# Performance work log

Hardware: AMD Instinct MI355X
Metric: run time of the kernel (lower is better)

Reference implementation:

```python
import jax, jax.numpy as jnp
import numpy as np

N = 40000; E = 640000; F_IN = 128; HID = 32; HEADS = 4; G = 64
NEG_SLOPE = 0.2; LN_EPS = 1e-5


def setup_inputs() -> dict:
    key = jax.random.key(0)
    ks = jax.random.split(key, 24)
    rn = lambda k, shape, s=0.1: jax.random.normal(k, shape, jnp.float32) * s
    d = {}
    d["x"] = jax.random.normal(ks[0], (N, F_IN), jnp.float32)
    d["edge_index"] = jax.random.randint(ks[1], (2, E), 0, N)
    d["batch"] = jnp.sort(jax.random.randint(ks[2], (N,), 0, G))
    # GAT layer 0: in F_IN -> HID per head, HEADS heads, concat
    d["W0"] = rn(ks[3], (F_IN, HEADS * HID))
    d["as0"] = rn(ks[4], (HEADS, HID)); d["ad0"] = rn(ks[5], (HEADS, HID))
    d["b0"] = jnp.zeros((HEADS * HID,), jnp.float32)
    d["ln0_g"] = jnp.ones((HEADS * HID,), jnp.float32); d["ln0_b"] = jnp.zeros((HEADS * HID,), jnp.float32)
    # GAT layer 1: HEADS*HID -> HID per head, HEADS heads, concat
    d["W1"] = rn(ks[6], (HEADS * HID, HEADS * HID))
    d["as1"] = rn(ks[7], (HEADS, HID)); d["ad1"] = rn(ks[8], (HEADS, HID))
    d["b1"] = jnp.zeros((HEADS * HID,), jnp.float32)
    d["ln1_g"] = jnp.ones((HEADS * HID,), jnp.float32); d["ln1_b"] = jnp.zeros((HEADS * HID,), jnp.float32)
    # GAT layer 2: HEADS*HID -> HID, 1 head, no concat
    d["W2"] = rn(ks[9], (HEADS * HID, HID))
    d["as2"] = rn(ks[10], (1, HID)); d["ad2"] = rn(ks[11], (1, HID))
    d["b2"] = jnp.zeros((HID,), jnp.float32)
    d["ln2_g"] = jnp.ones((HID,), jnp.float32); d["ln2_b"] = jnp.zeros((HID,), jnp.float32)
    # classifier: HID -> HID//2 -> 2
    d["fc1_w"] = rn(ks[12], (HID, HID // 2)); d["fc1_b"] = jnp.zeros((HID // 2,), jnp.float32)
    d["fc2_w"] = rn(ks[13], (HID // 2, 2)); d["fc2_b"] = jnp.zeros((2,), jnp.float32)
    return d


def gat_layer(x, src, dst, W, a_s, a_d, b, heads, out_c, concat):
    n = x.shape[0]
    h = (x @ W).reshape(n, heads, out_c)            # [N,H,C]
    al_s = jnp.sum(h * a_s, axis=-1)                # [N,H]
    al_d = jnp.sum(h * a_d, axis=-1)                # [N,H]
    e = jax.nn.leaky_relu(al_s[src] + al_d[dst], NEG_SLOPE)  # [E,H]
    m = jax.ops.segment_max(e, dst, num_segments=n)          # segment softmax over dst
    ex = jnp.exp(e - m[dst])
    s = jax.ops.segment_sum(ex, dst, num_segments=n)
    alpha = ex / (s[dst] + 1e-16)                   # [E,H]
    out = jax.ops.segment_sum(h[src] * alpha[:, :, None], dst, num_segments=n)  # [N,H,C]
    out = out.reshape(n, heads * out_c) if concat else out.mean(axis=1)
    return out + b


def layer_norm(x, g, b):
    mu = x.mean(-1, keepdims=True)
    var = jnp.var(x, axis=-1, keepdims=True)
    return (x - mu) * jax.lax.rsqrt(var + LN_EPS) * g + b


def reference(x, edge_index, batch, W0, as0, ad0, b0, ln0_g, ln0_b, W1, as1, ad1, b1, ln1_g, ln1_b, W2, as2, ad2, b2, ln2_g, ln2_b, fc1_w, fc1_b, fc2_w, fc2_b):
    src, dst = edge_index[0], edge_index[1]
    h = gat_layer(x, src, dst, W0, as0, ad0, b0, HEADS, HID, True)
    h = jax.nn.elu(layer_norm(h, ln0_g, ln0_b))
    h = gat_layer(h, src, dst, W1, as1, ad1, b1, HEADS, HID, True)
    h = jax.nn.elu(layer_norm(h, ln1_g, ln1_b))
    h = gat_layer(h, src, dst, W2, as2, ad2, b2, 1, HID, False)
    h = jax.nn.elu(layer_norm(h, ln2_g, ln2_b))
    cnt = jax.ops.segment_sum(jnp.ones((h.shape[0],), h.dtype), batch, num_segments=G)
    hg = jax.ops.segment_sum(h, batch, num_segments=G) / jnp.maximum(cnt, 1.0)[:, None]  # global mean pool [G,HID]
    z = jax.nn.relu(hg @ fc1_w + fc1_b)
    return z @ fc2_w + fc2_b
```

## Files before the change

kernel.cpp:

```cpp
#include <hip/hip_runtime.h>
#include <hip/hip_fp16.h>
#include <math.h>

#define NN 40000
#define EE 640000
#define NG 64
#define SCAN_BLOCKS ((NN + 1023) / 1024)

__device__ __forceinline__ float eluf(float x) { return x > 0.f ? x : expm1f(x); }

typedef const __attribute__((address_space(1))) char gas_char;
typedef __attribute__((address_space(3))) char las_char;

__device__ __forceinline__ void async_copy16(void* l, const void* g) {
  __builtin_amdgcn_global_load_lds((gas_char*)g, (las_char*)l, 16, 0, 0);
}

typedef __fp16 f16x2 __attribute__((ext_vector_type(2)));
__device__ __forceinline__ unsigned packh(float lo, float hi) {
  f16x2 p = __builtin_amdgcn_cvt_pkrtz(lo, hi);
  union { f16x2 h; unsigned u; } c; c.h = p; return c.u;
}
__device__ __forceinline__ float hlo(unsigned p) {
  union { unsigned u; f16x2 h; } c; c.u = p; return (float)c.h.x;
}
__device__ __forceinline__ float hhi(unsigned p) {
  union { unsigned u; f16x2 h; } c; c.u = p; return (float)c.h.y;
}

__global__ void zero_int_kernel(int* __restrict__ p, int n) {
  int i = blockIdx.x * 256 + threadIdx.x;
  if (i < n) p[i] = 0;
}

__global__ void count_deg_kernel(const int* __restrict__ dst, int* __restrict__ deg, int e) {
  int i = blockIdx.x * 256 + threadIdx.x;
  if (i < e) atomicAdd(&deg[dst[i]], 1);
}

__global__ __launch_bounds__(1024) void scanA_kernel(const int* __restrict__ deg,
                                                     int* __restrict__ row_ptr,
                                                     int* __restrict__ bsum, int n) {
  __shared__ int wsum[16];
  int t = threadIdx.x, lane = t & 63, wid = t >> 6;
  int i = blockIdx.x * 1024 + t;
  int v = (i < n) ? deg[i] : 0;
#pragma unroll
  for (int off = 1; off < 64; off <<= 1) {
    int u = __shfl_up(v, off);
    if (lane >= off) v += u;
  }
  if (lane == 63) wsum[wid] = v;
  __syncthreads();
  if (t < 16) {
    int w = wsum[t];
#pragma unroll
    for (int off = 1; off < 16; off <<= 1) {
      int u = __shfl_up(w, off);
      if (t >= off) w += u;
    }
    wsum[t] = w;
  }
  __syncthreads();
  if (wid > 0) v += wsum[wid - 1];
  if (i < n) row_ptr[i + 1] = v;
  if (t == 1023) bsum[blockIdx.x] = v;
}

__global__ void scanB_kernel(const int* __restrict__ bsum, int* __restrict__ boff, int nb) {
  int lane = threadIdx.x;
  int v = (lane < nb) ? bsum[lane] : 0;
  int orig = v;
#pragma unroll
  for (int off = 1; off < 64; off <<= 1) {
    int u = __shfl_up(v, off);
    if (lane >= off) v += u;
  }
  if (lane < nb) boff[lane] = v - orig;
}

__global__ __launch_bounds__(1024) void scanC_kernel(int* __restrict__ row_ptr,
                                                     const int* __restrict__ boff,
                                                     int* __restrict__ cursor, int n) {
  int i = blockIdx.x * 1024 + threadIdx.x;
  if (i < n) {
    int v = row_ptr[i + 1] + boff[i >> 10];
    row_ptr[i + 1] = v;
    if (i + 1 < n) cursor[i + 1] = v;
    if (i == 0) { cursor[0] = 0; row_ptr[0] = 0; }
  }
}

__global__ void scatter_kernel(const int* __restrict__ src, const int* __restrict__ dst,
                               int* __restrict__ cursor, int* __restrict__ csr_src, int e) {
  int i = blockIdx.x * 256 + threadIdx.x;
  if (i < e) {
    int d = dst[i];
    int pos = atomicAdd(&cursor[d], 1);
    csr_src[pos] = src[i];
  }
}

__global__ __launch_bounds__(256, 2) void gemm128_kernel(
    const float* __restrict__ x, const float* __restrict__ W,
    const float* __restrict__ a_s, const float* __restrict__ a_d,
    unsigned* __restrict__ hb, float* __restrict__ als, float* __restrict__ ald)
{
  __shared__ float xs[64 * 128];
  __shared__ float ws[2][32 * 128];

  int t = threadIdx.x;
  int row0 = blockIdx.x * 64;

  {
    const char* xg = (const char*)(x + (size_t)row0 * 128);
    char* xl = (char*)xs;
#pragma unroll
    for (int it = 0; it < 8; ++it)
      async_copy16(xl + it * 4096 + t * 16, xg + it * 4096 + t * 16);
  }
  {
    const char* wg = (const char*)W;
    char* wl = (char*)ws[0];
#pragma unroll
    for (int p = 0; p < 4; ++p)
      async_copy16(wl + p * 4096 + t * 16, wg + p * 4096 + t * 16);
  }
  __syncthreads();

  int cg = t & 31, rg = t >> 5;
  int r0 = rg * 8;
  int jlo = 2 * cg;

  float acc[8][4];
#pragma unroll
  for (int r = 0; r < 8; ++r)
#pragma unroll
    for (int c = 0; c < 4; ++c) acc[r][c] = 0.f;

  for (int ch = 0; ch < 4; ++ch) {
    if (ch < 3) {
      const char* wg = (const char*)W + (size_t)(ch + 1) * 32 * 128 * 4;
      char* wl = (char*)ws[(ch + 1) & 1];
#pragma unroll
      for (int p = 0; p < 4; ++p)
        async_copy16(wl + p * 4096 + t * 16, wg + p * 4096 + t * 16);
    }
    const float* wc = ws[ch & 1];
    const float* xc = xs + ch * 32;
#pragma unroll
    for (int kk = 0; kk < 32; kk += 4) {
      float2 wlo[4], whi[4];
#pragma unroll
      for (int q = 0; q < 4; ++q) {
        wlo[q] = *reinterpret_cast<const float2*>(&wc[(kk + q) * 128 + jlo]);
        whi[q] = *reinterpret_cast<const float2*>(&wc[(kk + q) * 128 + 64 + jlo]);
      }
#pragma unroll
      for (int r = 0; r < 8; ++r) {
        float4 xv = *reinterpret_cast<const float4*>(&xc[(r0 + r) * 128 + kk]);
        float a0 = acc[r][0], a1 = acc[r][1], a2 = acc[r][2], a3 = acc[r][3];
        a0 = fmaf(xv.x, wlo[0].x, a0); a1 = fmaf(xv.x, wlo[0].y, a1);
        a2 = fmaf(xv.x, whi[0].x, a2); a3 = fmaf(xv.x, whi[0].y, a3);
        a0 = fmaf(xv.y, wlo[1].x, a0); a1 = fmaf(xv.y, wlo[1].y, a1);
        a2 = fmaf(xv.y, whi[1].x, a2); a3 = fmaf(xv.y, whi[1].y, a3);
        a0 = fmaf(xv.z, wlo[2].x, a0); a1 = fmaf(xv.z, wlo[2].y, a1);
        a2 = fmaf(xv.z, whi[2].x, a2); a3 = fmaf(xv.z, whi[2].y, a3);
        a0 = fmaf(xv.w, wlo[3].x, a0); a1 = fmaf(xv.w, wlo[3].y, a1);
        a2 = fmaf(xv.w, whi[3].x, a2); a3 = fmaf(xv.w, whi[3].y, a3);
        acc[r][0] = a0; acc[r][1] = a1; acc[r][2] = a2; acc[r][3] = a3;
      }
    }
    __syncthreads();
  }

#pragma unroll
  for (int r = 0; r < 8; ++r) {
    uint2 pv;
    pv.x = packh(acc[r][0], acc[r][2]);
    pv.y = packh(acc[r][1], acc[r][3]);
    *reinterpret_cast<uint2*>(&hb[(size_t)(row0 + r0 + r) * 64 + jlo]) = pv;
  }

  float as0 = a_s[jlo], as1 = a_s[jlo + 1], as2 = a_s[jlo + 64], as3 = a_s[jlo + 65];
  float ad0 = a_d[jlo], ad1 = a_d[jlo + 1], ad2 = a_d[jlo + 64], ad3 = a_d[jlo + 65];
  int lane = t & 63;
#pragma unroll
  for (int r = 0; r < 8; ++r) {
    float psa = fmaf(acc[r][0], as0, acc[r][1] * as1);
    float psb = fmaf(acc[r][2], as2, acc[r][3] * as3);
    float pda = fmaf(acc[r][0], ad0, acc[r][1] * ad1);
    float pdb = fmaf(acc[r][2], ad2, acc[r][3] * ad3);
#pragma unroll
    for (int m = 1; m < 16; m <<= 1) {
      psa += __shfl_xor(psa, m); psb += __shfl_xor(psb, m);
      pda += __shfl_xor(pda, m); pdb += __shfl_xor(pdb, m);
    }
    if ((lane & 15) == 0) {
      int hA = (lane >> 4) & 1;
      size_t row = (size_t)(row0 + r0 + r);
      als[row * 4 + hA] = psa; als[row * 4 + hA + 2] = psb;
      ald[row * 4 + hA] = pda; ald[row * 4 + hA + 2] = pdb;
    }
  }
}

__global__ __launch_bounds__(256, 2) void gemm32_kernel(
    const float* __restrict__ x, const float* __restrict__ W,
    const float* __restrict__ a_s, const float* __restrict__ a_d,
    float* __restrict__ h, float* __restrict__ als, float* __restrict__ ald)
{
  __shared__ float xs[64 * 128];
  __shared__ float ws[2][32 * 32];
  int t = threadIdx.x;
  int row0 = blockIdx.x * 64;
  {
    const char* xg = (const char*)(x + (size_t)row0 * 128);
    char* xl = (char*)xs;
#pragma unroll
    for (int it = 0; it < 8; ++it)
      async_copy16(xl + it * 4096 + t * 16, xg + it * 4096 + t * 16);
  }
  async_copy16((char*)ws[0] + t * 16, (const char*)W + t * 16);
  __syncthreads();

  int cg = t & 7, rg = t >> 3;
  int r0 = rg * 2, c0 = cg * 4;
  float acc[2][4];
#pragma unroll
  for (int r = 0; r < 2; ++r)
#pragma unroll
    for (int c = 0; c < 4; ++c) acc[r][c] = 0.f;

  for (int ch = 0; ch < 4; ++ch) {
    if (ch < 3) {
      const char* wg = (const char*)W + (size_t)(ch + 1) * 32 * 32 * 4;
      async_copy16((char*)ws[(ch + 1) & 1] + t * 16, wg + t * 16);
    }
    const float* wc = ws[ch & 1];
    const float* xc = xs + ch * 32;
#pragma unroll
    for (int kk = 0; kk < 32; kk += 4) {
      float4 wv[4];
#pragma unroll
      for (int q = 0; q < 4; ++q)
        wv[q] = *reinterpret_cast<const float4*>(&wc[(kk + q) * 32 + c0]);
#pragma unroll
      for (int r = 0; r < 2; ++r) {
        float4 xv = *reinterpret_cast<const float4*>(&xc[(r0 + r) * 128 + kk]);
#pragma unroll
        for (int c = 0; c < 4; ++c) {
          float a = acc[r][c];
          a = fmaf(xv.x, (&wv[0].x)[c], a);
          a = fmaf(xv.y, (&wv[1].x)[c], a);
          a = fmaf(xv.z, (&wv[2].x)[c], a);
          a = fmaf(xv.w, (&wv[3].x)[c], a);
          acc[r][c] = a;
        }
      }
    }
    __syncthreads();
  }

#pragma unroll
  for (int r = 0; r < 2; ++r) {
    float4 hv = make_float4(acc[r][0], acc[r][1], acc[r][2], acc[r][3]);
    *reinterpret_cast<float4*>(&h[(size_t)(row0 + r0 + r) * 32 + c0]) = hv;
  }
  float asv[4], adv[4];
#pragma unroll
  for (int c = 0; c < 4; ++c) { asv[c] = a_s[c0 + c]; adv[c] = a_d[c0 + c]; }
#pragma unroll
  for (int r = 0; r < 2; ++r) {
    float ps = acc[r][0] * asv[0] + acc[r][1] * asv[1] + acc[r][2] * asv[2] + acc[r][3] * asv[3];
    float pd = acc[r][0] * adv[0] + acc[r][1] * adv[1] + acc[r][2] * adv[2] + acc[r][3] * adv[3];
#pragma unroll
    for (int m = 1; m < 8; m <<= 1) { ps += __shfl_xor(ps, m); pd += __shfl_xor(pd, m); }
    if ((t & 7) == 0) {
      als[row0 + r0 + r] = ps;
      ald[row0 + r0 + r] = pd;
    }
  }
}

__global__ __launch_bounds__(256) void aggregate128_kernel(
    const unsigned* __restrict__ hb, const float* __restrict__ als, const float* __restrict__ ald,
    const int* __restrict__ row_ptr, const int* __restrict__ csr_src,
    const float* __restrict__ bias, const float* __restrict__ ln_g, const float* __restrict__ ln_b,
    float* __restrict__ out, int n)
{
  __shared__ int s_src[4][64];
  __shared__ float s_ex[4][64][4];
  int t = threadIdx.x, lane = t & 63, wid = t >> 6;
  int node = blockIdx.x * 4 + wid;
  if (node >= n) return;
  int start = row_ptr[node], end = row_ptr[node + 1];
  int deg = end - start;

  float4 adq = reinterpret_cast<const float4*>(ald)[node];
  float adl[4] = {adq.x, adq.y, adq.z, adq.w};
  int hi = lane >> 5, c = lane & 31;
  int h0 = c >> 4, h1 = h0 + 2;
  float a0 = 0.f, a1 = 0.f, a2 = 0.f, a3 = 0.f;
  float ssum[4];

  if (deg <= 64) {
    bool valid = lane < deg;
    int s = 0;
    if (valid) s = csr_src[start + lane];
    float4 q = reinterpret_cast<const float4*>(als)[s];
    float v[4] = {q.x, q.y, q.z, q.w};
    float ex[4];
#pragma unroll
    for (int hh = 0; hh < 4; ++hh) {
      float w = v[hh] + adl[hh];
      w = w > 0.f ? w : 0.2f * w;
      ex[hh] = valid ? __expf(w) : 0.f;
      ssum[hh] = ex[hh];
    }
#pragma unroll
    for (int hh = 0; hh < 4; ++hh)
#pragma unroll
      for (int m = 1; m < 64; m <<= 1) ssum[hh] += __shfl_xor(ssum[hh], m);

    s_src[wid][lane] = s;
#pragma unroll
    for (int hh = 0; hh < 4; ++hh) s_ex[wid][lane][hh] = ex[hh];

    int d1 = deg >> 1, d0c = deg - d1;
    int base = hi ? d0c : 0;
    int cnt = hi ? d1 : d0c;
    float b0a = 0.f, b1a = 0.f, b2a = 0.f, b3a = 0.f;
    int j = 0;
    for (; j + 2 <= cnt; j += 2) {
      int sa = s_src[wid][base + j];
      int sb = s_src[wid][base + j + 1];
      uint2 ua = *reinterpret_cast<const uint2*>(&hb[(size_t)sa * 64 + 2 * c]);
      uint2 ub = *reinterpret_cast<const uint2*>(&hb[(size_t)sb * 64 + 2 * c]);
      float wa0 = s_ex[wid][base + j][h0], wa1 = s_ex[wid][base + j][h1];
      float wb0 = s_ex[wid][base + j + 1][h0], wb1 = s_ex[wid][base + j + 1][h1];
      a0 = fmaf(wa0, hlo(ua.x), a0); a1 = fmaf(wa0, hlo(ua.y), a1);
      a2 = fmaf(wa1, hhi(ua.x), a2); a3 = fmaf(wa1, hhi(ua.y), a3);
      b0a = fmaf(wb0, hlo(ub.x), b0a); b1a = fmaf(wb0, hlo(ub.y), b1a);
      b2a = fmaf(wb1, hhi(ub.x), b2a); b3a = fmaf(wb1, hhi(ub.y), b3a);
    }
    if (j < cnt) {
      int sa = s_src[wid][base + j];
      uint2 ua = *reinterpret_cast<const uint2*>(&hb[(size_t)sa * 64 + 2 * c]);
      float wa0 = s_ex[wid][base + j][h0], wa1 = s_ex[wid][base + j][h1];
      a0 = fmaf(wa0, hlo(ua.x), a0); a1 = fmaf(wa0, hlo(ua.y), a1);
      a2 = fmaf(wa1, hhi(ua.x), a2); a3 = fmaf(wa1, hhi(ua.y), a3);
    }
    a0 += b0a; a1 += b1a; a2 += b2a; a3 += b3a;
    a0 += __shfl_xor(a0, 32); a1 += __shfl_xor(a1, 32);
    a2 += __shfl_xor(a2, 32); a3 += __shfl_xor(a3, 32);
  } else {
#pragma unroll
    for (int hh = 0; hh < 4; ++hh) ssum[hh] = 0.f;
    for (int eb = start; eb < end; eb += 64) {
      int e = eb + lane;
      int s = 0;
      float exv[4] = {0.f, 0.f, 0.f, 0.f};
      if (e < end) {
        s = csr_src[e];
        float4 q = reinterpret_cast<const float4*>(als)[s];
        float av[4] = {q.x, q.y, q.z, q.w};
#pragma unroll
        for (int hh = 0; hh < 4; ++hh) {
          float v = av[hh] + adl[hh];
          v = v > 0.f ? v : 0.2f * v;
          exv[hh] = __expf(v);
          ssum[hh] += exv[hh];
        }
      }
      s_src[wid][lane] = s;
#pragma unroll
      for (int hh = 0; hh < 4; ++hh) s_ex[wid][lane][hh] = exv[hh];
      int cnt = end - eb; if (cnt > 64) cnt = 64;
      for (int j = 0; j < cnt; ++j) {
        int sj = s_src[wid][j];
        uint2 u = *reinterpret_cast<const uint2*>(&hb[(size_t)sj * 64 + 2 * c]);
        float w0 = s_ex[wid][j][h0], w1 = s_ex[wid][j][h1];
        a0 = fmaf(w0, hlo(u.x), a0); a1 = fmaf(w0, hlo(u.y), a1);
        a2 = fmaf(w1, hhi(u.x), a2); a3 = fmaf(w1, hhi(u.y), a3);
      }
    }
#pragma unroll
    for (int hh = 0; hh < 4; ++hh)
#pragma unroll
      for (int m = 1; m < 64; m <<= 1) ssum[hh] += __shfl_xor(ssum[hh], m);
    a0 *= 0.5f; a1 *= 0.5f; a2 *= 0.5f; a3 *= 0.5f;
    a0 += __shfl_xor(a0, 32); a1 += __shfl_xor(a1, 32);
    a2 += __shfl_xor(a2, 32); a3 += __shfl_xor(a3, 32);
  }

  float2 blo = *reinterpret_cast<const float2*>(&bias[2 * c]);
  float2 bhi = *reinterpret_cast<const float2*>(&bias[2 * c + 64]);
  float is0 = 1.f / (ssum[h0] + 1e-16f), is1 = 1.f / (ssum[h1] + 1e-16f);
  float o0 = a0 * is0 + blo.x;
  float o1 = a1 * is0 + blo.y;
  float o2 = a2 * is1 + bhi.x;
  float o3 = a3 * is1 + bhi.y;
  float red = o0 + o1 + o2 + o3;
  float sq2 = o0 * o0 + o1 * o1 + o2 * o2 + o3 * o3;
#pragma unroll
  for (int m = 1; m < 64; m <<= 1) {
    red += __shfl_xor(red, m);
    sq2 += __shfl_xor(sq2, m);
  }
  float mu = red * (1.f / 256.f);
  float var = sq2 * (1.f / 256.f) - mu * mu;
  float rstd = rsqrtf(var + 1e-5f);
  int f = 2 * c + 64 * hi;
  float2 gv = *reinterpret_cast<const float2*>(&ln_g[f]);
  float2 bv = *reinterpret_cast<const float2*>(&ln_b[f]);
  float dx = (hi ? o2 : o0) - mu, dy = (hi ? o3 : o1) - mu;
  float2 yv;
  yv.x = eluf(dx * rstd * gv.x + bv.x);
  yv.y = eluf(dy * rstd * gv.y + bv.y);
  *reinterpret_cast<float2*>(&out[(size_t)node * 128 + f]) = yv;
}

__global__ __launch_bounds__(256) void aggregate32_kernel(
    const float* __restrict__ h, const float* __restrict__ als, const float* __restrict__ ald,
    const int* __restrict__ row_ptr, const int* __restrict__ csr_src,
    const float* __restrict__ bias, const float* __restrict__ ln_g, const float* __restrict__ ln_b,
    float* __restrict__ out, int n)
{
  __shared__ int s_src[4][64];
  __shared__ float s_ex[4][64];
  int t = threadIdx.x, lane = t & 63, wid = t >> 6;
  int node = blockIdx.x * 4 + wid;
  if (node >= n) return;
  int start = row_ptr[node], end = row_ptr[node + 1];
  int deg = end - start;
  float adl = ald[node];
  int hi = lane >> 5, col = lane & 31;
  float acc0 = 0.f, ssum = 0.f;

  if (deg <= 64) {
    bool valid = lane < deg;
    int s = 0;
    if (valid) s = csr_src[start + lane];
    float v = als[s] + adl;
    v = v > 0.f ? v : 0.2f * v;
    float ex = valid ? __expf(v) : 0.f;
    ssum = ex;
#pragma unroll
    for (int m = 1; m < 64; m <<= 1) ssum += __shfl_xor(ssum, m);
    s_src[wid][lane] = s;
    s_ex[wid][lane] = ex;

    int d1 = deg >> 1, d0c = deg - d1;
    int base = hi ? d0c : 0;
    int cnt = hi ? d1 : d0c;
    float acc1 = 0.f;
    int j = 0;
    for (; j + 2 <= cnt; j += 2) {
      int sa = s_src[wid][base + j];
      int sb = s_src[wid][base + j + 1];
      float ha = h[(size_t)sa * 32 + col];
      float hbv = h[(size_t)sb * 32 + col];
      acc0 = fmaf(s_ex[wid][base + j], ha, acc0);
      acc1 = fmaf(s_ex[wid][base + j + 1], hbv, acc1);
    }
    if (j < cnt)
      acc0 = fmaf(s_ex[wid][base + j], h[(size_t)s_src[wid][base + j] * 32 + col], acc0);
    acc0 += acc1;
    acc0 += __shfl_xor(acc0, 32);
  } else {
    for (int eb = start; eb < end; eb += 64) {
      int e = eb + lane;
      int s = 0; float ex = 0.f;
      if (e < end) {
        s = csr_src[e];
        float v = als[s] + adl;
        v = v > 0.f ? v : 0.2f * v;
        ex = __expf(v);
        ssum += ex;
      }
      s_src[wid][lane] = s;
      s_ex[wid][lane] = ex;
      int cnt = end - eb; if (cnt > 64) cnt = 64;
      for (int j = 0; j < cnt; ++j)
        acc0 = fmaf(s_ex[wid][j], h[(size_t)s_src[wid][j] * 32 + col], acc0);
    }
#pragma unroll
    for (int m = 1; m < 64; m <<= 1) ssum += __shfl_xor(ssum, m);
    acc0 *= 0.5f;
    acc0 += __shfl_xor(acc0, 32);
  }

  float o0 = acc0 / (ssum + 1e-16f) + bias[col];
  float red = o0, sq2 = o0 * o0;
#pragma unroll
  for (int m = 1; m < 64; m <<= 1) {
    red += __shfl_xor(red, m);
    sq2 += __shfl_xor(sq2, m);
  }
  float mu = red * (1.f / 64.f);
  float var = sq2 * (1.f / 64.f) - mu * mu;
  float rstd = rsqrtf(var + 1e-5f);
  float y0 = (o0 - mu) * rstd * ln_g[col] + ln_b[col];
  if (lane < 32) out[(size_t)node * 32 + col] = eluf(y0);
}

__device__ __forceinline__ int lower_bound_dev(const int* a, int n, int key) {
  int lo = 0, hi = n;
  while (lo < hi) { int mid = (lo + hi) >> 1; if (a[mid] < key) lo = mid + 1; else hi = mid; }
  return lo;
}

__global__ __launch_bounds__(256) void poolfc_kernel(
    const float* __restrict__ x2, const int* __restrict__ batch,
    const float* __restrict__ fc1w, const float* __restrict__ fc1b,
    const float* __restrict__ fc2w, const float* __restrict__ fc2b,
    float* __restrict__ out, int n)
{
  int g = blockIdx.x;
  int lo = lower_bound_dev(batch, n, g);
  int hi = lower_bound_dev(batch, n, g + 1);
  int t = threadIdx.x;
  int c = t & 31, r = t >> 5;
  float acc = 0.f;
  for (int i = lo + r; i < hi; i += 8) acc += x2[(size_t)i * 32 + c];
  __shared__ float red[8][32];
  __shared__ float hgl[32];
  __shared__ float zl[16];
  red[r][c] = acc;
  __syncthreads();
  if (r == 0) {
    float s = 0.f;
#pragma unroll
    for (int k = 0; k < 8; ++k) s += red[k][c];
    float cnt = (float)(hi - lo);
    hgl[c] = s / fmaxf(cnt, 1.f);
  }
  __syncthreads();
  if (t < 16) {
    float a = fc1b[t];
#pragma unroll
    for (int k = 0; k < 32; ++k) a = fmaf(hgl[k], fc1w[k * 16 + t], a);
    zl[t] = fmaxf(a, 0.f);
  }
  __syncthreads();
  if (t < 2) {
    float a = fc2b[t];
#pragma unroll
    for (int j = 0; j < 16; ++j) a = fmaf(zl[j], fc2w[j * 2 + t], a);
    out[g * 2 + t] = a;
  }
}

extern "C" void kernel_launch(void* const* d_in, const int* in_sizes, int n_in,
                              void* d_out, int out_size, void* d_ws, size_t ws_size,
                              hipStream_t stream) {
  const float* x    = (const float*)d_in[0];
  const int*   ei   = (const int*)d_in[1];
  const int*   batch= (const int*)d_in[2];
  const float* W0   = (const float*)d_in[3];
  const float* as0  = (const float*)d_in[4];
  const float* ad0  = (const float*)d_in[5];
  const float* b0   = (const float*)d_in[6];
  const float* ln0g = (const float*)d_in[7];
  const float* ln0b = (const float*)d_in[8];
  const float* W1   = (const float*)d_in[9];
  const float* as1  = (const float*)d_in[10];
  const float* ad1  = (const float*)d_in[11];
  const float* b1   = (const float*)d_in[12];
  const float* ln1g = (const float*)d_in[13];
  const float* ln1b = (const float*)d_in[14];
  const float* W2   = (const float*)d_in[15];
  const float* as2  = (const float*)d_in[16];
  const float* ad2  = (const float*)d_in[17];
  const float* b2   = (const float*)d_in[18];
  const float* ln2g = (const float*)d_in[19];
  const float* ln2b = (const float*)d_in[20];
  const float* fc1w = (const float*)d_in[21];
  const float* fc1b = (const float*)d_in[22];
  const float* fc2w = (const float*)d_in[23];
  const float* fc2b = (const float*)d_in[24];
  float* out = (float*)d_out;

  const int* srce = ei;
  const int* dste = ei + EE;

  unsigned* hb = (unsigned*)d_ws;
  float* B2  = (float*)(hb + (size_t)NN * 64);
  float* als = B2 + (size_t)NN * 128;
  float* ald = als + (size_t)NN * 4;
  float* h2  = ald + (size_t)NN * 4;
  float* x2  = h2 + (size_t)NN * 32;
  int* deg      = (int*)(x2 + (size_t)NN * 32);
  int* row_ptr  = deg + NN;
  int* cursor   = row_ptr + NN + 1;
  int* csr_src  = cursor + NN;
  int* bsum     = csr_src + EE;
  int* boff     = bsum + SCAN_BLOCKS;

  zero_int_kernel<<<(NN + 255) / 256, 256, 0, stream>>>(deg, NN);
  count_deg_kernel<<<(EE + 255) / 256, 256, 0, stream>>>(dste, deg, EE);
  scanA_kernel<<<SCAN_BLOCKS, 1024, 0, stream>>>(deg, row_ptr, bsum, NN);
  scanB_kernel<<<1, 64, 0, stream>>>(bsum, boff, SCAN_BLOCKS);
  scanC_kernel<<<SCAN_BLOCKS, 1024, 0, stream>>>(row_ptr, boff, cursor, NN);
  scatter_kernel<<<(EE + 255) / 256, 256, 0, stream>>>(srce, dste, cursor, csr_src, EE);

  gemm128_kernel<<<625, 256, 0, stream>>>(x, W0, as0, ad0, hb, als, ald);
  aggregate128_kernel<<<(NN + 3) / 4, 256, 0, stream>>>(hb, als, ald, row_ptr, csr_src,
                                                        b0, ln0g, ln0b, B2, NN);
  gemm128_kernel<<<625, 256, 0, stream>>>(B2, W1, as1, ad1, hb, als, ald);
  aggregate128_kernel<<<(NN + 3) / 4, 256, 0, stream>>>(hb, als, ald, row_ptr, csr_src,
                                                        b1, ln1g, ln1b, B2, NN);
  gemm32_kernel<<<625, 256, 0, stream>>>(B2, W2, as2, ad2, h2, als, ald);
  aggregate32_kernel<<<(NN + 3) / 4, 256, 0, stream>>>(h2, als, ald, row_ptr, csr_src,
                                                       b2, ln2g, ln2b, x2, NN);
  poolfc_kernel<<<NG, 256, 0, stream>>>(x2, batch, fc1w, fc1b, fc2w, fc2b, out, NN);
}
```

Measured before the change: 278.0 us.

## Stream x tiles through double-buffered LDS and fold softmax sums into aggregation loops

```diff
diff --git a/kernel.cpp b/kernel.cpp
--- a/kernel.cpp
+++ b/kernel.cpp
@@ -101,30 +101,26 @@
   }
 }
 
-__global__ __launch_bounds__(256, 2) void gemm128_kernel(
+__global__ __launch_bounds__(256, 3) void gemm128_kernel(
     const float* __restrict__ x, const float* __restrict__ W,
     const float* __restrict__ a_s, const float* __restrict__ a_d,
     unsigned* __restrict__ hb, float* __restrict__ als, float* __restrict__ ald)
 {
-  __shared__ float xs[64 * 128];
+  __shared__ float xs[2][64 * 32];
   __shared__ float ws[2][32 * 128];
 
   int t = threadIdx.x;
   int row0 = blockIdx.x * 64;
+  const char* xgb = (const char*)x + (size_t)row0 * 512;
 
   {
-    const char* xg = (const char*)(x + (size_t)row0 * 128);
-    char* xl = (char*)xs;
-#pragma unroll
-    for (int it = 0; it < 8; ++it)
-      async_copy16(xl + it * 4096 + t * 16, xg + it * 4096 + t * 16);
-  }
-  {
+    int li0 = t, li1 = t + 256;
+    async_copy16((char*)xs[0] + li0 * 16, xgb + (li0 >> 3) * 512 + (li0 & 7) * 16);
+    async_copy16((char*)xs[0] + li1 * 16, xgb + (li1 >> 3) * 512 + (li1 & 7) * 16);
     const char* wg = (const char*)W;
-    char* wl = (char*)ws[0];
 #pragma unroll
     for (int p = 0; p < 4; ++p)
-      async_copy16(wl + p * 4096 + t * 16, wg + p * 4096 + t * 16);
+      async_copy16((char*)ws[0] + p * 4096 + t * 16, wg + p * 4096 + t * 16);
   }
   __syncthreads();
 
@@ -140,14 +136,18 @@
 
   for (int ch = 0; ch < 4; ++ch) {
     if (ch < 3) {
+      int b = (ch + 1) & 1;
+      int li0 = t, li1 = t + 256;
+      const char* xg = xgb + (ch + 1) * 128;
+      async_copy16((char*)xs[b] + li0 * 16, xg + (li0 >> 3) * 512 + (li0 & 7) * 16);
+      async_copy16((char*)xs[b] + li1 * 16, xg + (li1 >> 3) * 512 + (li1 & 7) * 16);
       const char* wg = (const char*)W + (size_t)(ch + 1) * 32 * 128 * 4;
-      char* wl = (char*)ws[(ch + 1) & 1];
 #pragma unroll
       for (int p = 0; p < 4; ++p)
-        async_copy16(wl + p * 4096 + t * 16, wg + p * 4096 + t * 16);
+        async_copy16((char*)ws[b] + p * 4096 + t * 16, wg + p * 4096 + t * 16);
     }
     const float* wc = ws[ch & 1];
-    const float* xc = xs + ch * 32;
+    const float* xc = xs[ch & 1];
 #pragma unroll
     for (int kk = 0; kk < 32; kk += 4) {
       float2 wlo[4], whi[4];
@@ -158,7 +158,7 @@
       }
 #pragma unroll
       for (int r = 0; r < 8; ++r) {
-        float4 xv = *reinterpret_cast<const float4*>(&xc[(r0 + r) * 128 + kk]);
+        float4 xv = *reinterpret_cast<const float4*>(&xc[(r0 + r) * 32 + kk]);
         float a0 = acc[r][0], a1 = acc[r][1], a2 = acc[r][2], a3 = acc[r][3];
         a0 = fmaf(xv.x, wlo[0].x, a0); a1 = fmaf(xv.x, wlo[0].y, a1);
         a2 = fmaf(xv.x, whi[0].x, a2); a3 = fmaf(xv.x, whi[0].y, a3);
@@ -290,7 +290,7 @@
     float* __restrict__ out, int n)
 {
   __shared__ int s_src[4][64];
-  __shared__ float s_ex[4][64][4];
+  __shared__ float2 s_w[4][64][2];
   int t = threadIdx.x, lane = t & 63, wid = t >> 6;
   int node = blockIdx.x * 4 + wid;
   if (node >= n) return;
@@ -300,14 +300,13 @@
   float4 adq = reinterpret_cast<const float4*>(ald)[node];
   float adl[4] = {adq.x, adq.y, adq.z, adq.w};
   int hi = lane >> 5, c = lane & 31;
-  int h0 = c >> 4, h1 = h0 + 2;
+  int hsel = c >> 4;
   float a0 = 0.f, a1 = 0.f, a2 = 0.f, a3 = 0.f;
-  float ssum[4];
+  float ssum0 = 0.f, ssum1 = 0.f;
 
   if (deg <= 64) {
-    bool valid = lane < deg;
     int s = 0;
-    if (valid) s = csr_src[start + lane];
+    if (lane < deg) s = csr_src[start + lane];
     float4 q = reinterpret_cast<const float4*>(als)[s];
     float v[4] = {q.x, q.y, q.z, q.w};
     float ex[4];
@@ -315,48 +314,46 @@
     for (int hh = 0; hh < 4; ++hh) {
       float w = v[hh] + adl[hh];
       w = w > 0.f ? w : 0.2f * w;
-      ex[hh] = valid ? __expf(w) : 0.f;
-      ssum[hh] = ex[hh];
-    }
-#pragma unroll
-    for (int hh = 0; hh < 4; ++hh)
-#pragma unroll
-      for (int m = 1; m < 64; m <<= 1) ssum[hh] += __shfl_xor(ssum[hh], m);
-
+      ex[hh] = __expf(w);
+    }
     s_src[wid][lane] = s;
-#pragma unroll
-    for (int hh = 0; hh < 4; ++hh) s_ex[wid][lane][hh] = ex[hh];
+    s_w[wid][lane][0] = make_float2(ex[0], ex[2]);
+    s_w[wid][lane][1] = make_float2(ex[1], ex[3]);
 
     int d1 = deg >> 1, d0c = deg - d1;
     int base = hi ? d0c : 0;
     int cnt = hi ? d1 : d0c;
     float b0a = 0.f, b1a = 0.f, b2a = 0.f, b3a = 0.f;
+    float sb0 = 0.f, sb1 = 0.f;
     int j = 0;
     for (; j + 2 <= cnt; j += 2) {
       int sa = s_src[wid][base + j];
       int sb = s_src[wid][base + j + 1];
       uint2 ua = *reinterpret_cast<const uint2*>(&hb[(size_t)sa * 64 + 2 * c]);
       uint2 ub = *reinterpret_cast<const uint2*>(&hb[(size_t)sb * 64 + 2 * c]);
-      float wa0 = s_ex[wid][base + j][h0], wa1 = s_ex[wid][base + j][h1];
-      float wb0 = s_ex[wid][base + j + 1][h0], wb1 = s_ex[wid][base + j + 1][h1];
-      a0 = fmaf(wa0, hlo(ua.x), a0); a1 = fmaf(wa0, hlo(ua.y), a1);
-      a2 = fmaf(wa1, hhi(ua.x), a2); a3 = fmaf(wa1, hhi(ua.y), a3);
-      b0a = fmaf(wb0, hlo(ub.x), b0a); b1a = fmaf(wb0, hlo(ub.y), b1a);
-      b2a = fmaf(wb1, hhi(ub.x), b2a); b3a = fmaf(wb1, hhi(ub.y), b3a);
+      float2 wa = s_w[wid][base + j][hsel];
+      float2 wb = s_w[wid][base + j + 1][hsel];
+      a0 = fmaf(wa.x, hlo(ua.x), a0); a1 = fmaf(wa.x, hlo(ua.y), a1);
+      a2 = fmaf(wa.y, hhi(ua.x), a2); a3 = fmaf(wa.y, hhi(ua.y), a3);
+      ssum0 += wa.x; ssum1 += wa.y;
+      b0a = fmaf(wb.x, hlo(ub.x), b0a); b1a = fmaf(wb.x, hlo(ub.y), b1a);
+      b2a = fmaf(wb.y, hhi(ub.x), b2a); b3a = fmaf(wb.y, hhi(ub.y), b3a);
+      sb0 += wb.x; sb1 += wb.y;
     }
     if (j < cnt) {
       int sa = s_src[wid][base + j];
       uint2 ua = *reinterpret_cast<const uint2*>(&hb[(size_t)sa * 64 + 2 * c]);
-      float wa0 = s_ex[wid][base + j][h0], wa1 = s_ex[wid][base + j][h1];
-      a0 = fmaf(wa0, hlo(ua.x), a0); a1 = fmaf(wa0, hlo(ua.y), a1);
-      a2 = fmaf(wa1, hhi(ua.x), a2); a3 = fmaf(wa1, hhi(ua.y), a3);
+      float2 wa = s_w[wid][base + j][hsel];
+      a0 = fmaf(wa.x, hlo(ua.x), a0); a1 = fmaf(wa.x, hlo(ua.y), a1);
+      a2 = fmaf(wa.y, hhi(ua.x), a2); a3 = fmaf(wa.y, hhi(ua.y), a3);
+      ssum0 += wa.x; ssum1 += wa.y;
     }
     a0 += b0a; a1 += b1a; a2 += b2a; a3 += b3a;
+    ssum0 += sb0; ssum1 += sb1;
     a0 += __shfl_xor(a0, 32); a1 += __shfl_xor(a1, 32);
     a2 += __shfl_xor(a2, 32); a3 += __shfl_xor(a3, 32);
+    ssum0 += __shfl_xor(ssum0, 32); ssum1 += __shfl_xor(ssum1, 32);
   } else {
-#pragma unroll
-    for (int hh = 0; hh < 4; ++hh) ssum[hh] = 0.f;
     for (int eb = start; eb < end; eb += 64) {
       int e = eb + lane;
       int s = 0;
@@ -370,33 +367,31 @@
           float v = av[hh] + adl[hh];
           v = v > 0.f ? v : 0.2f * v;
           exv[hh] = __expf(v);
-          ssum[hh] += exv[hh];
         }
       }
       s_src[wid][lane] = s;
-#pragma unroll
-      for (int hh = 0; hh < 4; ++hh) s_ex[wid][lane][hh] = exv[hh];
+      s_w[wid][lane][0] = make_float2(exv[0], exv[2]);
+      s_w[wid][lane][1] = make_float2(exv[1], exv[3]);
       int cnt = end - eb; if (cnt > 64) cnt = 64;
       for (int j = 0; j < cnt; ++j) {
         int sj = s_src[wid][j];
         uint2 u = *reinterpret_cast<const uint2*>(&hb[(size_t)sj * 64 + 2 * c]);
-        float w0 = s_ex[wid][j][h0], w1 = s_ex[wid][j][h1];
-        a0 = fmaf(w0, hlo(u.x), a0); a1 = fmaf(w0, hlo(u.y), a1);
-        a2 = fmaf(w1, hhi(u.x), a2); a3 = fmaf(w1, hhi(u.y), a3);
+        float2 w = s_w[wid][j][hsel];
+        a0 = fmaf(w.x, hlo(u.x), a0); a1 = fmaf(w.x, hlo(u.y), a1);
+        a2 = fmaf(w.y, hhi(u.x), a2); a3 = fmaf(w.y, hhi(u.y), a3);
+        ssum0 += w.x; ssum1 += w.y;
       }
     }
-#pragma unroll
-    for (int hh = 0; hh < 4; ++hh)
-#pragma unroll
-      for (int m = 1; m < 64; m <<= 1) ssum[hh] += __shfl_xor(ssum[hh], m);
     a0 *= 0.5f; a1 *= 0.5f; a2 *= 0.5f; a3 *= 0.5f;
+    ssum0 *= 0.5f; ssum1 *= 0.5f;
     a0 += __shfl_xor(a0, 32); a1 += __shfl_xor(a1, 32);
     a2 += __shfl_xor(a2, 32); a3 += __shfl_xor(a3, 32);
+    ssum0 += __shfl_xor(ssum0, 32); ssum1 += __shfl_xor(ssum1, 32);
   }
 
   float2 blo = *reinterpret_cast<const float2*>(&bias[2 * c]);
   float2 bhi = *reinterpret_cast<const float2*>(&bias[2 * c + 64]);
-  float is0 = 1.f / (ssum[h0] + 1e-16f), is1 = 1.f / (ssum[h1] + 1e-16f);
+  float is0 = 1.f / (ssum0 + 1e-16f), is1 = 1.f / (ssum1 + 1e-16f);
   float o0 = a0 * is0 + blo.x;
   float o1 = a1 * is0 + blo.y;
   float o2 = a2 * is1 + bhi.x;
@@ -439,35 +434,37 @@
   float acc0 = 0.f, ssum = 0.f;
 
   if (deg <= 64) {
-    bool valid = lane < deg;
     int s = 0;
-    if (valid) s = csr_src[start + lane];
+    if (lane < deg) s = csr_src[start + lane];
     float v = als[s] + adl;
     v = v > 0.f ? v : 0.2f * v;
-    float ex = valid ? __expf(v) : 0.f;
-    ssum = ex;
-#pragma unroll
-    for (int m = 1; m < 64; m <<= 1) ssum += __shfl_xor(ssum, m);
+    float ex = __expf(v);
     s_src[wid][lane] = s;
     s_ex[wid][lane] = ex;
 
     int d1 = deg >> 1, d0c = deg - d1;
     int base = hi ? d0c : 0;
     int cnt = hi ? d1 : d0c;
-    float acc1 = 0.f;
+    float acc1 = 0.f, ssum1 = 0.f;
     int j = 0;
     for (; j + 2 <= cnt; j += 2) {
       int sa = s_src[wid][base + j];
       int sb = s_src[wid][base + j + 1];
       float ha = h[(size_t)sa * 32 + col];
       float hbv = h[(size_t)sb * 32 + col];
-      acc0 = fmaf(s_ex[wid][base + j], ha, acc0);
-      acc1 = fmaf(s_ex[wid][base + j + 1], hbv, acc1);
-    }
-    if (j < cnt)
-      acc0 = fmaf(s_ex[wid][base + j], h[(size_t)s_src[wid][base + j] * 32 + col], acc0);
-    acc0 += acc1;
+      float wa = s_ex[wid][base + j];
+      float wb = s_ex[wid][base + j + 1];
+      acc0 = fmaf(wa, ha, acc0); ssum += wa;
+      acc1 = fmaf(wb, hbv, acc1); ssum1 += wb;
+    }
+    if (j < cnt) {
+      float wa = s_ex[wid][base + j];
+      acc0 = fmaf(wa, h[(size_t)s_src[wid][base + j] * 32 + col], acc0);
+      ssum += wa;
+    }
+    acc0 += acc1; ssum += ssum1;
     acc0 += __shfl_xor(acc0, 32);
+    ssum += __shfl_xor(ssum, 32);
   } else {
     for (int eb = start; eb < end; eb += 64) {
       int e = eb + lane;
@@ -477,18 +474,19 @@
         float v = als[s] + adl;
         v = v > 0.f ? v : 0.2f * v;
         ex = __expf(v);
-        ssum += ex;
       }
       s_src[wid][lane] = s;
       s_ex[wid][lane] = ex;
       int cnt = end - eb; if (cnt > 64) cnt = 64;
-      for (int j = 0; j < cnt; ++j)
-        acc0 = fmaf(s_ex[wid][j], h[(size_t)s_src[wid][j] * 32 + col], acc0);
-    }
-#pragma unroll
-    for (int m = 1; m < 64; m <<= 1) ssum += __shfl_xor(ssum, m);
-    acc0 *= 0.5f;
+      for (int j = 0; j < cnt; ++j) {
+        float w = s_ex[wid][j];
+        acc0 = fmaf(w, h[(size_t)s_src[wid][j] * 32 + col], acc0);
+        ssum += w;
+      }
+    }
+    acc0 *= 0.5f; ssum *= 0.5f;
     acc0 += __shfl_xor(acc0, 32);
+    ssum += __shfl_xor(ssum, 32);
   }
 
   float o0 = acc0 / (ssum + 1e-16f) + bias[col];
```

Result: faster. 270.0 us (-2.9%).
